# Optimization experiments

Hardware: AMD Instinct MI355X
Metric: run time of the kernel (lower is better)

## Reference

```python
import jax, jax.numpy as jnp
import numpy as np

DIM = 256      # channel dim
NW = 7         # n_win per side
HEADS = 8
TOPK = 4
KVW = 4        # kv_per_win (ada_avgpool output side)
EPS = 1e-6


def _dwconv(x, w, b):
    # depthwise conv, NHWC, 'SAME' == padding k//2 for odd kernels
    y = jax.lax.conv_general_dilated(
        x, w, (1, 1), 'SAME',
        dimension_numbers=('NHWC', 'HWIO', 'NHWC'),
        feature_group_count=x.shape[-1])
    return y + b


def _ln(x, g, b):
    mu = x.mean(-1, keepdims=True)
    var = ((x - mu) ** 2).mean(-1, keepdims=True)
    return (x - mu) * jax.lax.rsqrt(var + EPS) * g + b


def _bra(x, qkv_w, qkv_b, wo_w, wo_b, lepe_w, lepe_b):
    # BiLevelRoutingAttention, x: (n, H, W, C)
    n, H, W, C = x.shape
    hw, ww = H // NW, W // NW          # window size (8, 8)
    scale = C ** -0.5                   # qk_dim ** -0.5 (BiFormer uses full qk_dim)
    qkv = x @ qkv_w.T + qkv_b           # (n, H, W, 3C)
    # window partition: n (j hw) (i ww) c -> n (j i) hw ww c
    qkv_win = qkv.reshape(n, NW, hw, NW, ww, 3 * C)
    qkv_win = qkv_win.transpose(0, 1, 3, 2, 4, 5).reshape(n, NW * NW, hw, ww, 3 * C)
    q = qkv_win[..., :C]                # (n, p2, hw, ww, C)
    kv = qkv_win[..., C:]               # (n, p2, hw, ww, 2C)
    # --- window-level routing (q/k detached in torch; no fwd effect) ---
    q_win = q.mean((2, 3))              # (n, p2, C)
    k_win = kv[..., :C].mean((2, 3))    # (n, p2, C)
    logits = jnp.einsum('npc,nqc->npq', q_win * scale, k_win)
    _, idx = jax.lax.top_k(logits, TOPK)            # (n, p2, k)
    # --- kv downsample: adaptive avg pool (hw,ww)->(KVW,KVW), exact 2x2 mean here ---
    fh, fw = hw // KVW, ww // KVW
    kv_pix = kv.reshape(n, NW * NW, KVW, fh, KVW, fw, 2 * C).mean((3, 5))
    kv_pix = kv_pix.reshape(n, NW * NW, KVW * KVW, 2 * C)   # (n, p2, w2, 2C)
    # --- gather top-k windows' kv ---
    kv_sel = jax.vmap(lambda t, ix: t[ix])(kv_pix, idx)     # (n, p2, k, w2, 2C)
    cph = C // HEADS
    k_sel = kv_sel[..., :C].reshape(n, NW * NW, TOPK * KVW * KVW, HEADS, cph)
    v_sel = kv_sel[..., C:].reshape(n, NW * NW, TOPK * KVW * KVW, HEADS, cph)
    q_pix = q.reshape(n, NW * NW, hw * ww, HEADS, cph)
    # --- windowed attention over gathered tokens ---
    att = jnp.einsum('npqmc,npsmc->npmqs', q_pix * scale, k_sel)
    att = jax.nn.softmax(att, axis=-1)
    out = jnp.einsum('npmqs,npsmc->npqmc', att, v_sel)
    out = out.reshape(n, NW, NW, hw, ww, C).transpose(0, 1, 3, 2, 4, 5).reshape(n, H, W, C)
    # --- lepe: depthwise 5x5 on v over the full image ---
    v_img = qkv[..., 2 * C:]
    out = out + _dwconv(v_img, lepe_w, lepe_b)
    return out @ wo_w.T + wo_b


def setup_inputs() -> dict:
    key = jax.random.key(0)
    ks = jax.random.split(key, 8)
    C, s = DIM, 0.02
    p = {}
    p['x'] = jax.random.normal(ks[0], (16, C, 56, 56), jnp.float32)
    p['pos_w'] = jax.random.normal(ks[1], (3, 3, 1, C), jnp.float32) * s
    p['pos_b'] = jnp.zeros((C,), jnp.float32)
    p['ln1_g'] = jnp.ones((C,), jnp.float32)
    p['ln1_b'] = jnp.zeros((C,), jnp.float32)
    p['ln2_g'] = jnp.ones((C,), jnp.float32)
    p['ln2_b'] = jnp.zeros((C,), jnp.float32)
    p['qkv_w'] = jax.random.normal(ks[2], (3 * C, C), jnp.float32) * s
    p['qkv_b'] = jnp.zeros((3 * C,), jnp.float32)
    p['wo_w'] = jax.random.normal(ks[3], (C, C), jnp.float32) * s
    p['wo_b'] = jnp.zeros((C,), jnp.float32)
    p['lepe_w'] = jax.random.normal(ks[4], (5, 5, 1, C), jnp.float32) * s
    p['lepe_b'] = jnp.zeros((C,), jnp.float32)
    p['fc1_w'] = jax.random.normal(ks[5], (4 * C, C), jnp.float32) * s
    p['fc1_b'] = jnp.zeros((4 * C,), jnp.float32)
    p['fc2_w'] = jax.random.normal(ks[6], (C, 4 * C), jnp.float32) * s
    p['fc2_b'] = jnp.zeros((C,), jnp.float32)
    return p


def reference(x, pos_w, pos_b, ln1_g, ln1_b, ln2_g, ln2_b, qkv_w, qkv_b,
              wo_w, wo_b, lepe_w, lepe_b, fc1_w, fc1_b, fc2_w, fc2_b):
    xh = x.transpose(0, 2, 3, 1)                       # NCHW -> NHWC
    xh = xh + _dwconv(xh, pos_w, pos_b)                # pos embed (dw 3x3)
    xh = xh + _bra(_ln(xh, ln1_g, ln1_b), qkv_w, qkv_b, wo_w, wo_b, lepe_w, lepe_b)
    h = _ln(xh, ln2_g, ln2_b)
    h = jax.nn.gelu(h @ fc1_w.T + fc1_b, approximate=False)
    xh = xh + (h @ fc2_w.T + fc2_b)
    return xh.transpose(0, 3, 1, 2)                    # NHWC -> NCHW
```

## Files before the change

kernel.cpp:

```cpp
#include <hip/hip_runtime.h>
#include <math.h>

static constexpr int NIMG = 16;
static constexpr int TOK  = NIMG * 56 * 56;
static constexpr size_t TC = (size_t)TOK * 256;
static constexpr int PTOK = 784 * 16;

typedef __bf16 bf16x8 __attribute__((ext_vector_type(8)));
typedef float  f32x4  __attribute__((ext_vector_type(4)));

__device__ inline float bf2f(unsigned short u) {
  unsigned int i = ((unsigned int)u) << 16; float f; __builtin_memcpy(&f, &i, 4); return f;
}
__device__ inline unsigned short f2bf(float f) {
  unsigned int i; __builtin_memcpy(&i, &f, 4);
  unsigned int r = i + 0x7fffu + ((i >> 16) & 1u);
  return (unsigned short)(r >> 16);
}

__global__ __launch_bounds__(256) void nchw2nhwc(const float* __restrict__ x,
                                                 float* __restrict__ y) {
  __shared__ float T[32][37];
  int nh = blockIdx.z;
  int n = nh / 56, h = nh % 56;
  int c0 = blockIdx.y * 32, w0 = blockIdx.x * 32;
  int tid = threadIdx.x;
  int wlim = 56 - w0; if (wlim > 32) wlim = 32;
  {
    int ci = tid >> 3, w = (tid & 7) * 4;
    if (w < wlim) {
      f32x4 v = *(const f32x4*)&x[(((size_t)n * 256 + c0 + ci) * 56 + h) * 56 + w0 + w];
#pragma unroll
      for (int j = 0; j < 4; j++) T[ci][w + j] = v[j];
    }
  }
  __syncthreads();
  {
    int wi = tid >> 3, cq = tid & 7;
    if (wi < wlim) {
      f32x4 o;
#pragma unroll
      for (int k = 0; k < 4; k++) o[k] = T[cq * 4 + k][wi];
      *(f32x4*)&y[(((size_t)n * 56 + h) * 56 + w0 + wi) * 256 + c0 + cq * 4] = o;
    }
  }
}

__global__ __launch_bounds__(256) void posln_kernel(const float* __restrict__ xt,
                                                    const float* __restrict__ w,
                                                    const float* __restrict__ bb,
                                                    const float* __restrict__ g1,
                                                    const float* __restrict__ b1,
                                                    float* __restrict__ xh,
                                                    unsigned short* __restrict__ lnb,
                                                    float* __restrict__ murs) {
  int bid = blockIdx.x;
  int wgid = (bid & 7) * 1568 + (bid >> 3);
  int t = wgid * 4 + (threadIdx.x >> 6);
  int lane = threadIdx.x & 63;
  int c = lane * 4;
  int n = t / 3136, rem = t % 3136, h = rem / 56, ww = rem % 56;
  const float* base = xt + (size_t)n * 3136 * 256 + c;

  f32x4 xx[9]; float msk[9];
#pragma unroll
  for (int k = 0; k < 9; k++) {
    int dh = k / 3 - 1, dw = k % 3 - 1;
    int hh = h + dh, wc = ww + dw;
    msk[k] = ((unsigned)hh < 56u && (unsigned)wc < 56u) ? 1.f : 0.f;
    int hcl = hh < 0 ? 0 : (hh > 55 ? 55 : hh);
    int wcl = wc < 0 ? 0 : (wc > 55 ? 55 : wc);
    xx[k] = *(const f32x4*)&base[(size_t)(hcl * 56 + wcl) * 256];
  }
  f32x4 acc = *(const f32x4*)&bb[c];
#pragma unroll
  for (int k = 0; k < 9; k++) {
    f32x4 wv = *(const f32x4*)&w[k * 256 + c];
    acc += xx[k] * (wv * msk[k]);
  }
  f32x4 v = xx[4] + acc;
  *(f32x4*)&xh[(size_t)t * 256 + c] = v;

  float s = v[0] + v[1] + v[2] + v[3];
#pragma unroll
  for (int m = 1; m < 64; m <<= 1) s += __shfl_xor(s, m);
  float mu = s * (1.f / 256.f);
  f32x4 d = v - mu;
  float ss = d[0] * d[0] + d[1] * d[1] + d[2] * d[2] + d[3] * d[3];
#pragma unroll
  for (int m = 1; m < 64; m <<= 1) ss += __shfl_xor(ss, m);
  float rs = rsqrtf(ss * (1.f / 256.f) + 1e-6f);
  f32x4 gg = *(const f32x4*)&g1[c];
  f32x4 b4 = *(const f32x4*)&b1[c];
  f32x4 y = d * rs * gg + b4;
  unsigned short yb[4];
#pragma unroll
  for (int j = 0; j < 4; j++) yb[j] = f2bf(y[j]);
  __builtin_memcpy(lnb + (size_t)t * 256 + c, yb, 8);
  if (lane == 0) {
    murs[2 * (size_t)t] = mu;
    murs[2 * (size_t)t + 1] = rs;
  }
}

template <bool OUTBF, bool LN2F, bool NCHWOUT = false>
__global__ __launch_bounds__(512, 4) void mgemm2(const unsigned short* __restrict__ A, int lda,
                                                 const unsigned short* __restrict__ B, int ldb,
                                                 const float* __restrict__ bias,
                                                 const float* __restrict__ R,
                                                 void* __restrict__ C_,
                                                 int N, int K, int flags, int gx,
                                                 const float* __restrict__ g2,
                                                 const float* __restrict__ b2,
                                                 unsigned short* __restrict__ ob2) {
  __shared__ __attribute__((aligned(16))) char smraw[49152];
  unsigned short* As = (unsigned short*)smraw;
  unsigned short* Bs = (unsigned short*)(smraw + 16384);
  float* slab = (float*)smraw;
  constexpr int SSTR = 260;

  int tid = threadIdx.x;
  int nwg = gridDim.x, bid = blockIdx.x;
  int q8 = nwg >> 3, r8 = nwg & 7;
  int xcd = bid & 7, pos = bid >> 3;
  int wgid = (xcd < r8 ? xcd * (q8 + 1) : r8 * (q8 + 1) + (xcd - r8) * q8) + pos;
  int m0 = (wgid / gx) * 128;
  int n0 = (wgid % gx) * 256;

  int lane = tid & 63, wid = tid >> 6;
  int wr = (wid >> 2) * 64, wc = (wid & 3) * 64;
  int llo = lane & 15, lhi = lane >> 4;

  f32x4 acc[4][4];
#pragma unroll
  for (int i = 0; i < 4; i++)
#pragma unroll
    for (int j = 0; j < 4; j++) acc[i][j] = (f32x4){0.f, 0.f, 0.f, 0.f};

  for (int k0 = 0; k0 < K; k0 += 64) {
#pragma unroll
    for (int i = 0; i < 2; i++) {
      int qa = tid + 512 * i;
      int row = qa >> 3, col = (qa & 7) ^ (row & 7);
      __builtin_amdgcn_global_load_lds(
          (const __attribute__((address_space(1))) unsigned int*)
              (A + (size_t)(m0 + row) * lda + k0 + col * 8),
          (__attribute__((address_space(3))) unsigned int*)(As + qa * 8), 16, 0, 0);
    }
#pragma unroll
    for (int i = 0; i < 4; i++) {
      int qb = tid + 512 * i;
      int row = qb >> 3, col = (qb & 7) ^ (row & 7);
      __builtin_amdgcn_global_load_lds(
          (const __attribute__((address_space(1))) unsigned int*)
              (B + (size_t)(n0 + row) * ldb + k0 + col * 8),
          (__attribute__((address_space(3))) unsigned int*)(Bs + qb * 8), 16, 0, 0);
    }
    __syncthreads();
#pragma unroll
    for (int ks = 0; ks < 2; ks++) {
      int cchunk = ks * 4 + lhi;
      bf16x8 af[4], bfr[4];
#pragma unroll
      for (int mi = 0; mi < 4; mi++) {
        int r = wr + mi * 16 + llo;
        __builtin_memcpy(&af[mi], As + (size_t)r * 64 + (cchunk ^ (r & 7)) * 8, 16);
      }
#pragma unroll
      for (int nj = 0; nj < 4; nj++) {
        int r = wc + nj * 16 + llo;
        __builtin_memcpy(&bfr[nj], Bs + (size_t)r * 64 + (cchunk ^ (r & 7)) * 8, 16);
      }
#pragma unroll
      for (int mi = 0; mi < 4; mi++)
#pragma unroll
        for (int nj = 0; nj < 4; nj++)
          acc[mi][nj] = __builtin_amdgcn_mfma_f32_16x16x32_bf16(af[mi], bfr[nj],
                                                                acc[mi][nj], 0, 0, 0);
    }
    __syncthreads();
  }

#pragma unroll
  for (int s = 0; s < 4; s++) {
    if (wr == (s >> 1) * 64) {
#pragma unroll
      for (int mi2 = 0; mi2 < 2; mi2++) {
        int mi = (s & 1) * 2 + mi2;
#pragma unroll
        for (int nj = 0; nj < 4; nj++) {
          int col = wc + nj * 16 + llo;
#pragma unroll
          for (int j = 0; j < 4; j++)
            slab[(mi2 * 16 + lhi * 4 + j) * SSTR + col] = acc[mi][nj][j];
        }
      }
    }
    __syncthreads();
    int gmBase = m0 + s * 32;
    if (OUTBF) {
#pragma unroll
      for (int i2 = 0; i2 < 2; i2++) {
        int rr = wid * 4 + i2 * 2 + (lane >> 5);
        int col = (lane & 31) * 8;
        f32x4 v0 = *(f32x4*)&slab[rr * SSTR + col];
        f32x4 v1 = *(f32x4*)&slab[rr * SSTR + col + 4];
        if (!(flags & 8)) {
          v0 += *(const f32x4*)&bias[n0 + col];
          v1 += *(const f32x4*)&bias[n0 + col + 4];
        }
        if (flags & 1) {
#pragma unroll
          for (int j = 0; j < 4; j++) {
            v0[j] = 0.5f * v0[j] * (1.0f + erff(v0[j] * 0.70710678118654752f));
            v1[j] = 0.5f * v1[j] * (1.0f + erff(v1[j] * 0.70710678118654752f));
          }
        }
        unsigned short ob[8];
#pragma unroll
        for (int j = 0; j < 4; j++) { ob[j] = f2bf(v0[j]); ob[4 + j] = f2bf(v1[j]); }
        __builtin_memcpy((unsigned short*)C_ + (size_t)(gmBase + rr) * N + n0 + col, ob, 16);
      }
    } else {
#pragma unroll
      for (int i = 0; i < 4; i++) {
        int rr = wid * 4 + i;
        int gm = gmBase + rr;
        int col = lane * 4;
        f32x4 v = *(f32x4*)&slab[rr * SSTR + col];
        if (!(flags & 8)) v += *(const f32x4*)&bias[n0 + col];
        if (flags & 1) {
#pragma unroll
          for (int j = 0; j < 4; j++)
            v[j] = 0.5f * v[j] * (1.0f + erff(v[j] * 0.70710678118654752f));
        }
        if (flags & 2) v += *(const f32x4*)&R[(size_t)gm * N + n0 + col];
        if (LN2F) {
          float sv = v[0] + v[1] + v[2] + v[3];
          float qv = v[0] * v[0] + v[1] * v[1] + v[2] * v[2] + v[3] * v[3];
#pragma unroll
          for (int d = 1; d < 64; d <<= 1) {
            sv += __shfl_xor(sv, d);
            qv += __shfl_xor(qv, d);
          }
          float mu = sv * (1.f / 256.f);
          float var = qv * (1.f / 256.f) - mu * mu;
          float rs = rsqrtf(var + 1e-6f);
          f32x4 g4 = *(const f32x4*)&g2[col];
          f32x4 b4 = *(const f32x4*)&b2[col];
          f32x4 y = (v - mu) * rs * g4 + b4;
          unsigned short yb[4];
#pragma unroll
          for (int j = 0; j < 4; j++) yb[j] = f2bf(y[j]);
          __builtin_memcpy(ob2 + (size_t)gm * 256 + col, yb, 8);
        }
        if (NCHWOUT) {
          *(f32x4*)&slab[rr * SSTR + col] = v;
        } else {
          *(f32x4*)&((float*)C_)[(size_t)gm * N + n0 + col] = v;
        }
      }
      if (NCHWOUT) {
        __syncthreads();
        int n_img = gmBase / 3136;
        int hwb = gmBase % 3136;
        int c = tid & 255, half = tid >> 8;
        float* dst = (float*)C_ + ((size_t)n_img * 256 + c) * 3136 + hwb + half * 16;
#pragma unroll
        for (int i2 = 0; i2 < 4; i2++) {
          f32x4 v2;
#pragma unroll
          for (int j = 0; j < 4; j++)
            v2[j] = slab[(half * 16 + i2 * 4 + j) * SSTR + c];
          *(f32x4*)&dst[i2 * 4] = v2;
        }
      }
    }
    __syncthreads();
  }
}

__global__ __launch_bounds__(256) void prep_kernel(const float* __restrict__ qkv_w,
                                                   const float* __restrict__ qkv_b,
                                                   const float* __restrict__ wo_w,
                                                   const float* __restrict__ fc1_w,
                                                   const float* __restrict__ fc2_w,
                                                   const float* __restrict__ lepe_w,
                                                   unsigned short* __restrict__ wqv,
                                                   unsigned short* __restrict__ wkv,
                                                   unsigned short* __restrict__ wwo,
                                                   unsigned short* __restrict__ wfc1,
                                                   unsigned short* __restrict__ wfc2,
                                                   float* __restrict__ bqv,
                                                   unsigned short* __restrict__ wlep) {
  int i = blockIdx.x * 256 + threadIdx.x;
  if (i < 65536) { wqv[i] = f2bf(qkv_w[i]); }
  else if (i < 131072) { int j = i - 65536; wqv[65536 + j] = f2bf(qkv_w[512 * 256 + j]); }
  else if (i < 262144) { int j = i - 131072; wkv[j] = f2bf(qkv_w[256 * 256 + j]); }
  else if (i < 327680) { int j = i - 262144; wwo[j] = f2bf(wo_w[j]); }
  else if (i < 589824) { int j = i - 327680; wfc1[j] = f2bf(fc1_w[j]); }
  else if (i < 851968) { int j = i - 589824; wfc2[j] = f2bf(fc2_w[j]); }
  else if (i < 852480) { int j = i - 851968; bqv[j] = qkv_b[j < 256 ? j : j + 256]; }
  else if (i < 858880) { int j = i - 852480; wlep[j] = f2bf(lepe_w[j]); }
}

__global__ __launch_bounds__(256) void pool_kernel(const float* __restrict__ xh,
                                                   const float* __restrict__ murs,
                                                   const float* __restrict__ g1,
                                                   const float* __restrict__ b1,
                                                   unsigned short* __restrict__ plx,
                                                   float* __restrict__ wmx) {
  int np = blockIdx.x * 4 + (threadIdx.x >> 6);
  int lane = threadIdx.x & 63;
  int c = lane * 4;
  int n = np / 49, p = np % 49, wr = p / 7, wcq = p % 7;
  f32x4 g4 = *(const f32x4*)&g1[c];
  f32x4 b4 = *(const f32x4*)&b1[c];
  f32x4 tot = (f32x4){0.f, 0.f, 0.f, 0.f};
  for (int s = 0; s < 16; s++) {
    int i = s >> 2, j = s & 3;
    f32x4 z = (f32x4){0.f, 0.f, 0.f, 0.f};
    for (int di = 0; di < 2; di++)
      for (int dj = 0; dj < 2; dj++) {
        size_t t = ((size_t)n * 56 + wr * 8 + i * 2 + di) * 56 + wcq * 8 + j * 2 + dj;
        float mu = murs[2 * t], rs = murs[2 * t + 1];
        f32x4 v = *(const f32x4*)&xh[t * 256 + c];
        z += (v - mu) * rs;
      }
    z *= 0.25f;
    f32x4 cell = z * g4 + b4;
    unsigned short ab[4];
#pragma unroll
    for (int k = 0; k < 4; k++) ab[k] = f2bf(cell[k]);
    __builtin_memcpy(plx + ((size_t)np * 16 + s) * 256 + c, ab, 8);
    tot += z;
  }
  f32x4 wm = tot * (1.f / 16.f) * g4 + b4;
  *(f32x4*)&wmx[(size_t)np * 256 + c] = wm;
}

__global__ __launch_bounds__(256) void winproj_kernel(const float* __restrict__ wmx,
                                                      const float* __restrict__ qkv_w,
                                                      const float* __restrict__ qkv_b,
                                                      float* __restrict__ qkwin) {
  int np = blockIdx.x, t = threadIdx.x;
  __shared__ float xs[256];
  xs[t] = wmx[(size_t)np * 256 + t];
  __syncthreads();
  for (int rep = 0; rep < 2; rep++) {
    int n = t + rep * 256;
    const float* wrow = qkv_w + (size_t)n * 256;
    float s = qkv_b[n];
    for (int c = 0; c < 256; c++) s += xs[c] * wrow[c];
    qkwin[(size_t)np * 512 + n] = s;
  }
}

__global__ __launch_bounds__(64) void topk_kernel(const float* __restrict__ qkwin,
                                                  int* __restrict__ idx) {
  int np = blockIdx.x;
  int n = np / 49;
  int j = threadIdx.x;
  __shared__ float lg[49];
  if (j < 49) {
    const float* qp = qkwin + (size_t)np * 512;
    const float* kp = qkwin + ((size_t)n * 49 + j) * 512 + 256;
    float s = 0.f;
    for (int c = 0; c < 256; c++) s += qp[c] * kp[c];
    lg[j] = s;
  }
  __syncthreads();
  if (j == 0) {
    unsigned long long used = 0ull;
    for (int t = 0; t < 4; t++) {
      float best = -INFINITY;
      int bi = 0;
      for (int q = 0; q < 49; q++)
        if (!((used >> q) & 1ull) && lg[q] > best) { best = lg[q]; bi = q; }
      idx[np * 4 + t] = bi;
      used |= (1ull << bi);
    }
  }
}

__global__ __launch_bounds__(64) void attn_mfma(const unsigned short* __restrict__ qvb,
                                                const unsigned short* __restrict__ kvp,
                                                const int* __restrict__ idx,
                                                unsigned short* __restrict__ out) {
  __shared__ unsigned short Vt[32 * 72];
  __shared__ unsigned short Pl[64 * 72];
  int bid = blockIdx.x;
  int head = bid & 7, np = bid >> 3;
  int n = np / 49, p = np % 49;
  int h0 = (p / 7) * 8, w0 = (p % 7) * 8;
  int lane = threadIdx.x;
  int lhi = lane >> 4, llo = lane & 15;

  int wi4[4];
#pragma unroll
  for (int t = 0; t < 4; t++) wi4[t] = idx[np * 4 + t];

#pragma unroll
  for (int it = 0; it < 4; it++) {
    int cell = lane >> 2;
    int chunk = lane & 3;
    int s = it * 16 + cell;
    const unsigned short* g = kvp + ((size_t)(n * 49 + wi4[it]) * 16 + cell) * 512
                              + 256 + head * 32 + chunk * 8;
    unsigned short vv[8];
    __builtin_memcpy(vv, g, 16);
#pragma unroll
    for (int j = 0; j < 8; j++) Vt[(chunk * 8 + j) * 72 + s] = vv[j];
  }

  bf16x8 qf[4], kf[4];
#pragma unroll
  for (int mi = 0; mi < 4; mi++) {
    int row = mi * 16 + llo;
    int h = h0 + (row >> 3), w = w0 + (row & 7);
    __builtin_memcpy(&qf[mi],
                     qvb + (((size_t)n * 56 + h) * 56 + w) * 512 + head * 32 + lhi * 8, 16);
  }
#pragma unroll
  for (int nj = 0; nj < 4; nj++) {
    __builtin_memcpy(&kf[nj],
                     kvp + ((size_t)(n * 49 + wi4[nj]) * 16 + llo) * 512 + head * 32 + lhi * 8,
                     16);
  }

  f32x4 acc[4][4];
#pragma unroll
  for (int mi = 0; mi < 4; mi++)
#pragma unroll
    for (int nj = 0; nj < 4; nj++) acc[mi][nj] = (f32x4){0.f, 0.f, 0.f, 0.f};
#pragma unroll
  for (int mi = 0; mi < 4; mi++)
#pragma unroll
    for (int nj = 0; nj < 4; nj++)
      acc[mi][nj] = __builtin_amdgcn_mfma_f32_16x16x32_bf16(qf[mi], kf[nj], acc[mi][nj], 0, 0, 0);

#pragma unroll
  for (int mi = 0; mi < 4; mi++)
#pragma unroll
    for (int nj = 0; nj < 4; nj++) acc[mi][nj] *= 0.0625f;
#pragma unroll
  for (int mi = 0; mi < 4; mi++) {
#pragma unroll
    for (int reg = 0; reg < 4; reg++) {
      float m = fmaxf(fmaxf(acc[mi][0][reg], acc[mi][1][reg]),
                      fmaxf(acc[mi][2][reg], acc[mi][3][reg]));
      m = fmaxf(m, __shfl_xor(m, 1));
      m = fmaxf(m, __shfl_xor(m, 2));
      m = fmaxf(m, __shfl_xor(m, 4));
      m = fmaxf(m, __shfl_xor(m, 8));
      float sum = 0.f;
#pragma unroll
      for (int nj = 0; nj < 4; nj++) {
        float e = __expf(acc[mi][nj][reg] - m);
        acc[mi][nj][reg] = e;
        sum += e;
      }
      sum += __shfl_xor(sum, 1);
      sum += __shfl_xor(sum, 2);
      sum += __shfl_xor(sum, 4);
      sum += __shfl_xor(sum, 8);
      float inv = 1.0f / sum;
#pragma unroll
      for (int nj = 0; nj < 4; nj++) acc[mi][nj][reg] *= inv;
    }
  }

#pragma unroll
  for (int mi = 0; mi < 4; mi++)
#pragma unroll
    for (int nj = 0; nj < 4; nj++)
#pragma unroll
      for (int reg = 0; reg < 4; reg++) {
        int row = mi * 16 + lhi * 4 + reg;
        Pl[row * 72 + nj * 16 + llo] = f2bf(acc[mi][nj][reg]);
      }

  f32x4 o[4][2];
#pragma unroll
  for (int mi = 0; mi < 4; mi++)
#pragma unroll
    for (int nc = 0; nc < 2; nc++) o[mi][nc] = (f32x4){0.f, 0.f, 0.f, 0.f};
#pragma unroll
  for (int ks = 0; ks < 2; ks++) {
    bf16x8 pa[4], vb[2];
#pragma unroll
    for (int mi = 0; mi < 4; mi++)
      __builtin_memcpy(&pa[mi], Pl + (mi * 16 + llo) * 72 + ks * 32 + lhi * 8, 16);
#pragma unroll
    for (int nc = 0; nc < 2; nc++)
      __builtin_memcpy(&vb[nc], Vt + (nc * 16 + llo) * 72 + ks * 32 + lhi * 8, 16);
#pragma unroll
    for (int mi = 0; mi < 4; mi++)
#pragma unroll
      for (int nc = 0; nc < 2; nc++)
        o[mi][nc] = __builtin_amdgcn_mfma_f32_16x16x32_bf16(pa[mi], vb[nc], o[mi][nc], 0, 0, 0);
  }

  __syncthreads();
#pragma unroll
  for (int mi = 0; mi < 4; mi++)
#pragma unroll
    for (int nc = 0; nc < 2; nc++)
#pragma unroll
      for (int reg = 0; reg < 4; reg++) {
        int row = mi * 16 + lhi * 4 + reg;
        Pl[row * 40 + nc * 16 + llo] = f2bf(o[mi][nc][reg]);
      }
  __syncthreads();
#pragma unroll
  for (int it = 0; it < 4; it++) {
    int slot = it * 64 + lane;
    int row = slot >> 2, cp = slot & 3;
    unsigned short ov[8];
    __builtin_memcpy(ov, Pl + row * 40 + cp * 8, 16);
    int h = h0 + (row >> 3), w = w0 + (row & 7);
    __builtin_memcpy(out + (((size_t)n * 56 + h) * 56 + w) * 256 + head * 32 + cp * 8, ov, 16);
  }
}

__global__ __launch_bounds__(256) void lepe_kernel(const unsigned short* __restrict__ qvb,
                                                   const unsigned short* __restrict__ wlep,
                                                   const float* __restrict__ b,
                                                   unsigned short* __restrict__ out) {
  __shared__ unsigned short Vs[60 * 272];
  int bid = blockIdx.x;
  int wgid = (bid & 7) * 784 + (bid >> 3);
  int tb = wgid * 8;
  int n = tb / 3136, rem = tb % 3136;
  int h0 = rem / 56, w0 = rem % 56;
  int tid = threadIdx.x;

  const unsigned short* vimg = qvb + (size_t)n * 3136 * 512 + 256;
  {
    int chunk = tid & 31;
    for (int s = tid >> 5; s < 60; s += 8) {
      int r = s / 12, cc = s % 12;
      int hh = h0 + r - 2; hh = hh < 0 ? 0 : (hh > 55 ? 55 : hh);
      int wcg = w0 + cc - 2; wcg = wcg < 0 ? 0 : (wcg > 55 ? 55 : wcg);
      unsigned short tmp[8];
      __builtin_memcpy(tmp, vimg + (size_t)(hh * 56 + wcg) * 512 + chunk * 8, 16);
      __builtin_memcpy(&Vs[s * 272 + chunk * 8], tmp, 16);
    }
  }
  __syncthreads();

  int px = tid >> 5;
  int cg = tid & 31;
  int c = cg * 8;
  int wq = w0 + px;

  float acc[8];
#pragma unroll
  for (int j = 0; j < 8; j++) acc[j] = b[c + j];

#pragma unroll
  for (int r = 0; r < 5; r++) {
    float hok = ((unsigned)(h0 + r - 2) < 56u) ? 1.f : 0.f;
#pragma unroll
    for (int dc = 0; dc < 5; dc++) {
      float m = hok * (((unsigned)(wq + dc - 2) < 56u) ? 1.f : 0.f);
      int slot = r * 12 + px + dc;
      unsigned short vv[8], wv[8];
      __builtin_memcpy(vv, &Vs[slot * 272 + cg * 8], 16);
      __builtin_memcpy(wv, wlep + (r * 5 + dc) * 256 + c, 16);
#pragma unroll
      for (int j = 0; j < 8; j++) acc[j] += bf2f(vv[j]) * (bf2f(wv[j]) * m);
    }
  }

  size_t o = (size_t)(tb + px) * 256 + c;
  unsigned short ov[8];
  __builtin_memcpy(ov, out + o, 16);
  unsigned short nv[8];
#pragma unroll
  for (int j = 0; j < 8; j++) nv[j] = f2bf(bf2f(ov[j]) + acc[j]);
  __builtin_memcpy(out + o, nv, 16);
}

extern "C" void kernel_launch(void* const* d_in, const int* in_sizes, int n_in,
                              void* d_out, int out_size, void* d_ws, size_t ws_size,
                              hipStream_t stream) {
  const float* x      = (const float*)d_in[0];
  const float* pos_w  = (const float*)d_in[1];
  const float* pos_b  = (const float*)d_in[2];
  const float* ln1_g  = (const float*)d_in[3];
  const float* ln1_b  = (const float*)d_in[4];
  const float* ln2_g  = (const float*)d_in[5];
  const float* ln2_b  = (const float*)d_in[6];
  const float* qkv_w  = (const float*)d_in[7];
  const float* qkv_b  = (const float*)d_in[8];
  const float* wo_w   = (const float*)d_in[9];
  const float* wo_b   = (const float*)d_in[10];
  const float* lepe_w = (const float*)d_in[11];
  const float* lepe_b = (const float*)d_in[12];
  const float* fc1_w  = (const float*)d_in[13];
  const float* fc1_b  = (const float*)d_in[14];
  const float* fc2_w  = (const float*)d_in[15];
  const float* fc2_b  = (const float*)d_in[16];

  float*          xt   = (float*)d_out;
  unsigned short* qvb  = (unsigned short*)d_out;
  unsigned short* hbuf = (unsigned short*)d_out;

  float*          r2   = (float*)d_ws;
  float*          wmx  = r2 + TC;
  float*          qkw  = wmx + (size_t)784 * 256;
  float*          bqv  = qkw + (size_t)784 * 512;
  unsigned short* lnb  = (unsigned short*)(bqv + 512);
  unsigned short* aob  = lnb;
  unsigned short* ln2b = lnb;
  unsigned short* plx  = lnb + TC;
  unsigned short* kvp  = plx + (size_t)PTOK * 256;
  unsigned short* wqv  = kvp + (size_t)PTOK * 512;
  unsigned short* wkv  = wqv + (size_t)512 * 256;
  unsigned short* wwo  = wkv + (size_t)512 * 256;
  unsigned short* wfc1 = wwo + (size_t)256 * 256;
  unsigned short* wfc2 = wfc1 + (size_t)1024 * 256;
  int*            idx  = (int*)(wfc2 + (size_t)256 * 1024);
  float*          murs = (float*)(idx + 784 * 4);
  unsigned short* wlep = (unsigned short*)(murs + (size_t)TOK * 2);
  unsigned short* hfull = wlep + 6400;

  size_t base_bytes = (size_t)((char*)hfull - (char*)d_ws);
  bool fullmlp = ws_size >= base_bytes + (size_t)TOK * 1024 * 2;

  prep_kernel<<<3355, 256, 0, stream>>>(qkv_w, qkv_b, wo_w, fc1_w, fc2_w, lepe_w,
                                        wqv, wkv, wwo, wfc1, wfc2, bqv, wlep);
  nchw2nhwc<<<dim3(2, 8, NIMG * 56), 256, 0, stream>>>(x, xt);
  posln_kernel<<<TOK / 4, 256, 0, stream>>>(xt, pos_w, pos_b, ln1_g, ln1_b,
                                            r2, lnb, murs);
  pool_kernel<<<196, 256, 0, stream>>>(r2, murs, ln1_g, ln1_b, plx, wmx);
  mgemm2<true, false><<<784, 512, 0, stream>>>(lnb, 256, wqv, 256, bqv, nullptr,
                                               qvb, 512, 256, 0, 2,
                                               nullptr, nullptr, nullptr);
  mgemm2<true, false><<<196, 512, 0, stream>>>(plx, 256, wkv, 256, qkv_b + 256, nullptr,
                                               kvp, 512, 256, 0, 2,
                                               nullptr, nullptr, nullptr);
  winproj_kernel<<<784, 256, 0, stream>>>(wmx, qkv_w, qkv_b, qkw);
  topk_kernel<<<784, 64, 0, stream>>>(qkw, idx);
  attn_mfma<<<6272, 64, 0, stream>>>(qvb, kvp, idx, aob);
  lepe_kernel<<<TOK / 8, 256, 0, stream>>>(qvb, wlep, lepe_b, aob);
  mgemm2<false, true><<<392, 512, 0, stream>>>(aob, 256, wwo, 256, wo_b, r2,
                                               r2, 256, 256, 2, 1,
                                               ln2_g, ln2_b, ln2b);
  if (fullmlp) {
    mgemm2<true, false><<<1568, 512, 0, stream>>>(ln2b, 256, wfc1, 256, fc1_b, nullptr,
                                                  hfull, 1024, 256, 1, 4,
                                                  nullptr, nullptr, nullptr);
    mgemm2<false, false, true><<<392, 512, 0, stream>>>(hfull, 1024, wfc2, 1024, fc2_b, r2,
                                                        d_out, 256, 1024, 2, 1,
                                                        nullptr, nullptr, nullptr);
  } else {
    mgemm2<true, false><<<784, 512, 0, stream>>>(ln2b, 256, wfc1, 256, fc1_b, nullptr,
                                                 hbuf, 512, 256, 1, 2,
                                                 nullptr, nullptr, nullptr);
    mgemm2<false, false><<<392, 512, 0, stream>>>(hbuf, 512, wfc2, 1024, fc2_b, r2,
                                                  r2, 256, 512, 2, 1,
                                                  nullptr, nullptr, nullptr);
    mgemm2<true, false><<<784, 512, 0, stream>>>(ln2b, 256, wfc1 + (size_t)512 * 256, 256,
                                                 fc1_b + 512, nullptr,
                                                 hbuf, 512, 256, 1, 2,
                                                 nullptr, nullptr, nullptr);
    mgemm2<false, false, true><<<392, 512, 0, stream>>>(hbuf, 512, wfc2 + 512, 1024, fc2_b, r2,
                                                        d_out, 256, 512, 2 | 8, 1,
                                                        nullptr, nullptr, nullptr);
  }
}
```

Measured before the change: 431.2 us.

## Double-buffer GEMM k-tiles in LDS with 32-wide k steps

The main bf16 GEMM loop moves from single-buffered 64-wide k tiles to double-buffered 32-wide k tiles. Each step issues global-to-LDS loads for the next tile before running MFMAs on the current one, so memory latency can overlap compute and one barrier per step is dropped. In exchange there are twice as many loop iterations and barriers per unit of K, and a narrower swizzle (4 chunks). The async LDS loads are not explicitly waited on before the barrier, so correctness depends on the compiler inserting the vmcnt wait.

```diff
diff --git a/kernel.cpp b/kernel.cpp
--- a/kernel.cpp
+++ b/kernel.cpp
@@ -114,8 +114,6 @@
                                                  const float* __restrict__ b2,
                                                  unsigned short* __restrict__ ob2) {
   __shared__ __attribute__((aligned(16))) char smraw[49152];
-  unsigned short* As = (unsigned short*)smraw;
-  unsigned short* Bs = (unsigned short*)(smraw + 16384);
   float* slab = (float*)smraw;
   constexpr int SSTR = 260;
 
@@ -137,48 +135,55 @@
 #pragma unroll
     for (int j = 0; j < 4; j++) acc[i][j] = (f32x4){0.f, 0.f, 0.f, 0.f};
 
-  for (int k0 = 0; k0 < K; k0 += 64) {
-#pragma unroll
-    for (int i = 0; i < 2; i++) {
-      int qa = tid + 512 * i;
-      int row = qa >> 3, col = (qa & 7) ^ (row & 7);
-      __builtin_amdgcn_global_load_lds(
-          (const __attribute__((address_space(1))) unsigned int*)
-              (A + (size_t)(m0 + row) * lda + k0 + col * 8),
-          (__attribute__((address_space(3))) unsigned int*)(As + qa * 8), 16, 0, 0);
-    }
-#pragma unroll
-    for (int i = 0; i < 4; i++) {
-      int qb = tid + 512 * i;
-      int row = qb >> 3, col = (qb & 7) ^ (row & 7);
-      __builtin_amdgcn_global_load_lds(
-          (const __attribute__((address_space(1))) unsigned int*)
-              (B + (size_t)(n0 + row) * ldb + k0 + col * 8),
-          (__attribute__((address_space(3))) unsigned int*)(Bs + qb * 8), 16, 0, 0);
-    }
+  int arow = tid >> 2, ach = tid & 3;
+  int acs = ach ^ (arow & 3);
+  int brow0 = tid >> 2,          bch0 = tid & 3,          bcs0 = bch0 ^ (brow0 & 3);
+  int brow1 = (tid + 512) >> 2,  bch1 = tid & 3,          bcs1 = bch1 ^ (brow1 & 3);
+
+  auto STAGE = [&](int buf, int k0) {
+    unsigned short* Asb = (unsigned short*)(smraw + buf * 24576);
+    unsigned short* Bsb = Asb + 4096;
+    __builtin_amdgcn_global_load_lds(
+        (const __attribute__((address_space(1))) unsigned int*)
+            (A + (size_t)(m0 + arow) * lda + k0 + acs * 8),
+        (__attribute__((address_space(3))) unsigned int*)(Asb + tid * 8), 16, 0, 0);
+    __builtin_amdgcn_global_load_lds(
+        (const __attribute__((address_space(1))) unsigned int*)
+            (B + (size_t)(n0 + brow0) * ldb + k0 + bcs0 * 8),
+        (__attribute__((address_space(3))) unsigned int*)(Bsb + tid * 8), 16, 0, 0);
+    __builtin_amdgcn_global_load_lds(
+        (const __attribute__((address_space(1))) unsigned int*)
+            (B + (size_t)(n0 + brow1) * ldb + k0 + bcs1 * 8),
+        (__attribute__((address_space(3))) unsigned int*)(Bsb + (tid + 512) * 8), 16, 0, 0);
+  };
+
+  int NT = K >> 5;
+  STAGE(0, 0);
+  __syncthreads();
+  int cur = 0;
+  for (int kt = 0; kt < NT; kt++) {
+    if (kt + 1 < NT) STAGE(cur ^ 1, (kt + 1) * 32);
+    unsigned short* Asb = (unsigned short*)(smraw + cur * 24576);
+    unsigned short* Bsb = Asb + 4096;
+    bf16x8 af[4], bfr[4];
+#pragma unroll
+    for (int mi = 0; mi < 4; mi++) {
+      int r = wr + mi * 16 + llo;
+      __builtin_memcpy(&af[mi], Asb + (size_t)r * 32 + (lhi ^ (r & 3)) * 8, 16);
+    }
+#pragma unroll
+    for (int nj = 0; nj < 4; nj++) {
+      int r = wc + nj * 16 + llo;
+      __builtin_memcpy(&bfr[nj], Bsb + (size_t)r * 32 + (lhi ^ (r & 3)) * 8, 16);
+    }
+#pragma unroll
+    for (int mi = 0; mi < 4; mi++)
+#pragma unroll
+      for (int nj = 0; nj < 4; nj++)
+        acc[mi][nj] = __builtin_amdgcn_mfma_f32_16x16x32_bf16(af[mi], bfr[nj],
+                                                              acc[mi][nj], 0, 0, 0);
     __syncthreads();
-#pragma unroll
-    for (int ks = 0; ks < 2; ks++) {
-      int cchunk = ks * 4 + lhi;
-      bf16x8 af[4], bfr[4];
-#pragma unroll
-      for (int mi = 0; mi < 4; mi++) {
-        int r = wr + mi * 16 + llo;
-        __builtin_memcpy(&af[mi], As + (size_t)r * 64 + (cchunk ^ (r & 7)) * 8, 16);
-      }
-#pragma unroll
-      for (int nj = 0; nj < 4; nj++) {
-        int r = wc + nj * 16 + llo;
-        __builtin_memcpy(&bfr[nj], Bs + (size_t)r * 64 + (cchunk ^ (r & 7)) * 8, 16);
-      }
-#pragma unroll
-      for (int mi = 0; mi < 4; mi++)
-#pragma unroll
-        for (int nj = 0; nj < 4; nj++)
-          acc[mi][nj] = __builtin_amdgcn_mfma_f32_16x16x32_bf16(af[mi], bfr[nj],
-                                                                acc[mi][nj], 0, 0, 0);
-    }
-    __syncthreads();
+    cur ^= 1;
   }
 
 #pragma unroll
@@ -192,7 +197,7 @@
           int col = wc + nj * 16 + llo;
 #pragma unroll
           for (int j = 0; j < 4; j++)
-            slab[(mi2 * 16 + lhi * 4 + j) * SSTR + col] = acc[mi][nj][j];
+            slab[(mi2 * 16 + (lane >> 4) * 4 + j) * SSTR + col] = acc[mi][nj][j];
         }
       }
     }
```

Measured after the change: 452.4 us. 4.9% more time.

## Fuse NCHW-to-NHWC transpose into positional conv and LayerNorm kernel

Applied to the files above, without the earlier changes.

Removes the separate transpose kernel and has the pos-embed depthwise conv plus LN1 read the NCHW input directly. Each block handles one image row, each thread does 64 channels of one pixel, and the LN statistics are reduced across four lanes. This drops a full float write and read of the transposed tensor. In exchange, reads from NCHW are strided per thread (lanes differ in w and channel group), so coalescing may be poor. Variance now comes from E[x^2]-mu^2 rather than two passes, and xh is re-read from global memory for normalisation.

```diff
diff --git a/kernel.cpp b/kernel.cpp
--- a/kernel.cpp
+++ b/kernel.cpp
@@ -18,88 +18,92 @@
   return (unsigned short)(r >> 16);
 }
 
-__global__ __launch_bounds__(256) void nchw2nhwc(const float* __restrict__ x,
-                                                 float* __restrict__ y) {
-  __shared__ float T[32][37];
-  int nh = blockIdx.z;
-  int n = nh / 56, h = nh % 56;
-  int c0 = blockIdx.y * 32, w0 = blockIdx.x * 32;
+__global__ __launch_bounds__(256) void poslnT_kernel(const float* __restrict__ x,
+                                                     const float* __restrict__ w,
+                                                     const float* __restrict__ bb,
+                                                     const float* __restrict__ g1,
+                                                     const float* __restrict__ b1,
+                                                     float* __restrict__ xh,
+                                                     unsigned short* __restrict__ lnb,
+                                                     float* __restrict__ murs) {
+  int bid = blockIdx.x;
+  int wgid = (bid & 7) * 112 + (bid >> 3);
+  int n = wgid / 56, h = wgid % 56;
   int tid = threadIdx.x;
-  int wlim = 56 - w0; if (wlim > 32) wlim = 32;
-  {
-    int ci = tid >> 3, w = (tid & 7) * 4;
-    if (w < wlim) {
-      f32x4 v = *(const f32x4*)&x[(((size_t)n * 256 + c0 + ci) * 56 + h) * 56 + w0 + w];
-#pragma unroll
-      for (int j = 0; j < 4; j++) T[ci][w + j] = v[j];
-    }
-  }
-  __syncthreads();
-  {
-    int wi = tid >> 3, cq = tid & 7;
-    if (wi < wlim) {
-      f32x4 o;
-#pragma unroll
-      for (int k = 0; k < 4; k++) o[k] = T[cq * 4 + k][wi];
-      *(f32x4*)&y[(((size_t)n * 56 + h) * 56 + w0 + wi) * 256 + c0 + cq * 4] = o;
-    }
-  }
-}
-
-__global__ __launch_bounds__(256) void posln_kernel(const float* __restrict__ xt,
-                                                    const float* __restrict__ w,
-                                                    const float* __restrict__ bb,
-                                                    const float* __restrict__ g1,
-                                                    const float* __restrict__ b1,
-                                                    float* __restrict__ xh,
-                                                    unsigned short* __restrict__ lnb,
-                                                    float* __restrict__ murs) {
-  int bid = blockIdx.x;
-  int wgid = (bid & 7) * 1568 + (bid >> 3);
-  int t = wgid * 4 + (threadIdx.x >> 6);
-  int lane = threadIdx.x & 63;
-  int c = lane * 4;
-  int n = t / 3136, rem = t % 3136, h = rem / 56, ww = rem % 56;
-  const float* base = xt + (size_t)n * 3136 * 256 + c;
-
-  f32x4 xx[9]; float msk[9];
-#pragma unroll
-  for (int k = 0; k < 9; k++) {
-    int dh = k / 3 - 1, dw = k % 3 - 1;
-    int hh = h + dh, wc = ww + dw;
-    msk[k] = ((unsigned)hh < 56u && (unsigned)wc < 56u) ? 1.f : 0.f;
-    int hcl = hh < 0 ? 0 : (hh > 55 ? 55 : hh);
-    int wcl = wc < 0 ? 0 : (wc > 55 ? 55 : wc);
-    xx[k] = *(const f32x4*)&base[(size_t)(hcl * 56 + wcl) * 256];
-  }
-  f32x4 acc = *(const f32x4*)&bb[c];
-#pragma unroll
-  for (int k = 0; k < 9; k++) {
-    f32x4 wv = *(const f32x4*)&w[k * 256 + c];
-    acc += xx[k] * (wv * msk[k]);
-  }
-  f32x4 v = xx[4] + acc;
-  *(f32x4*)&xh[(size_t)t * 256 + c] = v;
-
-  float s = v[0] + v[1] + v[2] + v[3];
-#pragma unroll
-  for (int m = 1; m < 64; m <<= 1) s += __shfl_xor(s, m);
-  float mu = s * (1.f / 256.f);
-  f32x4 d = v - mu;
-  float ss = d[0] * d[0] + d[1] * d[1] + d[2] * d[2] + d[3] * d[3];
-#pragma unroll
-  for (int m = 1; m < 64; m <<= 1) ss += __shfl_xor(ss, m);
-  float rs = rsqrtf(ss * (1.f / 256.f) + 1e-6f);
-  f32x4 gg = *(const f32x4*)&g1[c];
-  f32x4 b4 = *(const f32x4*)&b1[c];
-  f32x4 y = d * rs * gg + b4;
-  unsigned short yb[4];
-#pragma unroll
-  for (int j = 0; j < 4; j++) yb[j] = f2bf(y[j]);
-  __builtin_memcpy(lnb + (size_t)t * 256 + c, yb, 8);
-  if (lane == 0) {
-    murs[2 * (size_t)t] = mu;
-    murs[2 * (size_t)t + 1] = rs;
+  int ww = tid >> 2;
+  int q = tid & 3;
+  bool act = ww < 56;
+  int wcl = act ? ww : 55;
+
+  const float* ximg = x + (size_t)n * 256 * 3136;
+  int hm = h > 0 ? h - 1 : 0, hp = h < 55 ? h + 1 : 55;
+  float mh0 = h > 0 ? 1.f : 0.f, mh2 = h < 55 ? 1.f : 0.f;
+  int wm = wcl > 0 ? wcl - 1 : 0, wp = wcl < 55 ? wcl + 1 : 55;
+  float mw0 = wcl > 0 ? 1.f : 0.f, mw2 = wcl < 55 ? 1.f : 0.f;
+
+  size_t t = ((size_t)n * 56 + h) * 56 + wcl;
+  float psum = 0.f, psq = 0.f;
+
+#pragma unroll
+  for (int cc = 0; cc < 8; cc++) {
+    float vv[8];
+#pragma unroll
+    for (int j = 0; j < 8; j++) {
+      int c = cc * 32 + q * 8 + j;
+      const float* xc = ximg + (size_t)c * 3136;
+      const float* r0 = xc + hm * 56;
+      const float* r1 = xc + h * 56;
+      const float* r2p = xc + hp * 56;
+      float a = bb[c];
+      a += r0[wm]  * (w[0 * 256 + c] * (mh0 * mw0));
+      a += r0[wcl] * (w[1 * 256 + c] * mh0);
+      a += r0[wp]  * (w[2 * 256 + c] * (mh0 * mw2));
+      a += r1[wm]  * (w[3 * 256 + c] * mw0);
+      float ctr = r1[wcl];
+      a += ctr * w[4 * 256 + c];
+      a += r1[wp]  * (w[5 * 256 + c] * mw2);
+      a += r2p[wm]  * (w[6 * 256 + c] * (mh2 * mw0));
+      a += r2p[wcl] * (w[7 * 256 + c] * mh2);
+      a += r2p[wp]  * (w[8 * 256 + c] * (mh2 * mw2));
+      float v = ctr + a;
+      vv[j] = v;
+      psum += v;
+      psq += v * v;
+    }
+    if (act) {
+      int c = cc * 32 + q * 8;
+      f32x4 v0 = (f32x4){vv[0], vv[1], vv[2], vv[3]};
+      f32x4 v1 = (f32x4){vv[4], vv[5], vv[6], vv[7]};
+      *(f32x4*)&xh[t * 256 + c] = v0;
+      *(f32x4*)&xh[t * 256 + c + 4] = v1;
+    }
+  }
+
+  psum += __shfl_xor(psum, 1); psum += __shfl_xor(psum, 2);
+  psq  += __shfl_xor(psq, 1);  psq  += __shfl_xor(psq, 2);
+  float mu = psum * (1.f / 256.f);
+  float var = psq * (1.f / 256.f) - mu * mu;
+  float rs = rsqrtf(var + 1e-6f);
+
+  if (act) {
+#pragma unroll
+    for (int cc = 0; cc < 8; cc++) {
+      int c = cc * 32 + q * 8;
+      f32x4 v0 = *(const f32x4*)&xh[t * 256 + c];
+      f32x4 v1 = *(const f32x4*)&xh[t * 256 + c + 4];
+      f32x4 g0 = *(const f32x4*)&g1[c], g4 = *(const f32x4*)&g1[c + 4];
+      f32x4 b0 = *(const f32x4*)&b1[c], b4 = *(const f32x4*)&b1[c + 4];
+      f32x4 y0 = (v0 - mu) * rs * g0 + b0;
+      f32x4 y1 = (v1 - mu) * rs * g4 + b4;
+      unsigned short yb[8];
+#pragma unroll
+      for (int j = 0; j < 4; j++) { yb[j] = f2bf(y0[j]); yb[4 + j] = f2bf(y1[j]); }
+      __builtin_memcpy(lnb + t * 256 + c, yb, 16);
+    }
+    if (q == 0) {
+      murs[2 * t] = mu;
+      murs[2 * t + 1] = rs;
+    }
   }
 }
 
@@ -603,7 +607,6 @@
   const float* fc2_w  = (const float*)d_in[15];
   const float* fc2_b  = (const float*)d_in[16];
 
-  float*          xt   = (float*)d_out;
   unsigned short* qvb  = (unsigned short*)d_out;
   unsigned short* hbuf = (unsigned short*)d_out;
 
@@ -631,9 +634,8 @@
 
   prep_kernel<<<3355, 256, 0, stream>>>(qkv_w, qkv_b, wo_w, fc1_w, fc2_w, lepe_w,
                                         wqv, wkv, wwo, wfc1, wfc2, bqv, wlep);
-  nchw2nhwc<<<dim3(2, 8, NIMG * 56), 256, 0, stream>>>(x, xt);
-  posln_kernel<<<TOK / 4, 256, 0, stream>>>(xt, pos_w, pos_b, ln1_g, ln1_b,
-                                            r2, lnb, murs);
+  poslnT_kernel<<<896, 256, 0, stream>>>(x, pos_w, pos_b, ln1_g, ln1_b,
+                                         r2, lnb, murs);
   pool_kernel<<<196, 256, 0, stream>>>(r2, murs, ln1_g, ln1_b, plx, wmx);
   mgemm2<true, false><<<784, 512, 0, stream>>>(lnb, 256, wqv, 256, bqv, nullptr,
                                                qvb, 512, 256, 0, 2,
```

After: 486.9 us. 12.9% more time.
